# Optimization experiments

Measured on AMD Instinct MI355X. Metric: run time of the kernel, lower is better.

The kernel has to match this reference:

```python
import jax, jax.numpy as jnp
import numpy as np

B, T, D, HS = 4, 4096, 512, 64


def setup_inputs() -> dict:
    key = jax.random.key(0)
    kx, kd, kk, kq, kv = jax.random.split(key, 5)
    X = jax.random.normal(kx, (B, T, D), dtype=jnp.float32)
    dag = jax.random.randint(kd, (T, T), 0, 2, dtype=jnp.int32)
    scale = 1.0 / np.sqrt(D).astype(np.float32)
    Wk = jax.random.normal(kk, (D, HS), dtype=jnp.float32) * scale
    Wq = jax.random.normal(kq, (D, HS), dtype=jnp.float32) * scale
    Wv = jax.random.normal(kv, (D, HS), dtype=jnp.float32) * scale
    return {"X": X, "dag": dag, "Wk": Wk, "Wq": Wq, "Wv": Wv}


def reference(X, dag, Wk, Wq, Wv):
    # Projections (nn.Linear without bias): [B,T,HS]
    K = X @ Wk
    Q = X @ Wq
    V = X @ Wv
    hs = Q.shape[-1]
    # Dense scores [B,T,T]
    QK = jnp.einsum('bid,bjd->bij', Q, K) / np.float32(np.sqrt(hs))
    mask = (dag == 0)  # [T,T], True -> -inf
    # Rows fully masked would softmax to NaN in torch; the module zeroes them.
    row_dead = jnp.all(mask, axis=-1)  # [T]
    neg_inf = jnp.asarray(-jnp.inf, QK.dtype)
    scores = jnp.where(mask, neg_inf, QK)
    # Neutralize dead rows before softmax to avoid NaN, then zero them out
    scores = jnp.where(row_dead[:, None], jnp.zeros((), QK.dtype), scores)
    att = jax.nn.softmax(scores, axis=-1)
    att = jnp.where(row_dead[:, None], jnp.zeros((), att.dtype), att)
    # Transposed AV matmul: out[b,j,h] = sum_i att[b,i,j] * V[b,i,h]
    out = jnp.einsum('bij,bih->bjh', att, V)
    # Swish activation
    return out * jax.nn.sigmoid(out)
```

## Files before the change

kernel.cpp:

```cpp
#include <hip/hip_runtime.h>
#include <hip/hip_bf16.h>
#include <math.h>

#define BB 4
#define TT 4096
#define DD 512
#define HH 64
#define TW 128

typedef unsigned int u32;
typedef unsigned short u16;
typedef float f32x16 __attribute__((ext_vector_type(16)));
typedef __bf16 bf16x8 __attribute__((ext_vector_type(8)));

#define SC 0.18033688011112042f

static __device__ __forceinline__ u16 f2b(float f) {
    __hip_bfloat16 h = __float2bfloat16(f);
    return __builtin_bit_cast(u16, h);
}
static __device__ __forceinline__ float b2f(u16 x) {
    return __builtin_bit_cast(float, (u32)x << 16);
}
static __device__ __forceinline__ u32 pk2(float a, float b) {
    return (u32)f2b(a) | ((u32)f2b(b) << 16);
}
static __device__ __forceinline__ bf16x8 ldf(const u16* p) {
    uint4 u = *(const uint4*)p;
    return __builtin_bit_cast(bf16x8, u);
}
static __device__ __forceinline__ void swap32(u32& a, u32& b) {
    asm("v_permlane32_swap_b32 %0, %1" : "+v"(a), "+v"(b));
}


__global__ __launch_bounds__(256) void wtr_kernel(const float* __restrict__ Wq,
                                                  const float* __restrict__ Wk,
                                                  const float* __restrict__ Wv,
                                                  u16* __restrict__ Wt) {
    const int wb = blockIdx.x;
    const int m = wb >> 3, sub = wb & 7;
    const float* W = (m == 0) ? Wq : (m == 1) ? Wk : Wv;
    const int t = threadIdx.x;
    const int n = sub * 8 + (t >> 5);
    const int k0 = (t & 31) * 16;
    u16 buf[16];
#pragma unroll
    for (int k = 0; k < 16; ++k) buf[k] = f2b(W[(size_t)(k0 + k) * HH + n]);
    uint4* dst = (uint4*)(Wt + ((size_t)m * 64 + n) * DD + k0);
    dst[0] = *(uint4*)buf;
    dst[1] = *(uint4*)(buf + 8);
}

__global__ __launch_bounds__(384) void pp_kernel(const float* __restrict__ X,
                                                 const u16* __restrict__ Wt,
                                                 u16* __restrict__ QF,
                                                 u16* __restrict__ KF,
                                                 u16* __restrict__ VF,
                                                 const int* __restrict__ dag,
                                                 u32* __restrict__ bits2,
                                                 u32* __restrict__ bitsTT) {
    if (blockIdx.x >= 256) {
        const int w = threadIdx.x >> 6, lane = threadIdx.x & 63;
        const int unit = (blockIdx.x - 256) * 6 + w;
        if (unit >= 8192) return;
        const int i32r = unit >> 6;
        const int j64 = unit & 63;
        const int i0 = i32r * 32, j0 = j64 * 64;
        const int* p = dag + (size_t)i0 * TT + j0 + lane;
        u32* b2lo = bits2 + (size_t)(j64 * 2) * TT + i0;
        u32* b2hi = bits2 + (size_t)(j64 * 2 + 1) * TT + i0;
        int vals[32];
#pragma unroll
        for (int r = 0; r < 32; ++r) vals[r] = p[(size_t)r * TT];
        u32 colw = 0;
#pragma unroll
        for (int r = 0; r < 32; ++r) {
            unsigned long long m = __ballot(vals[r] != 0);
            colw |= (vals[r] != 0 ? 1u : 0u) << r;
            if (lane == 0) b2lo[r] = (u32)m;
            else if (lane == 32) b2hi[r] = (u32)(m >> 32);
        }
        bitsTT[(size_t)i32r * TT + j0 + lane] = colw;
        return;
    }
    const int w = threadIdx.x >> 6, lane = threadIdx.x & 63;
    const int m = w % 3, rg = w / 3;
    const int l31 = lane & 31, hf = lane >> 5;
    const int tile = blockIdx.x * 2 + rg;
    const int row0 = tile * 32;
    const float* xr = X + (size_t)(row0 + l31) * DD + hf * 8;
    const u16* wbase = Wt + (size_t)m * 64 * DD + hf * 8;

    f32x16 acc[2] = {};

    for (int kt = 0; kt < 32; ++kt) {
        float4 x0 = *(const float4*)(xr + kt * 16);
        float4 x1 = *(const float4*)(xr + kt * 16 + 4);
        uint4 aw;
        aw.x = pk2(x0.x, x0.y);
        aw.y = pk2(x0.z, x0.w);
        aw.z = pk2(x1.x, x1.y);
        aw.w = pk2(x1.z, x1.w);
        bf16x8 xa = __builtin_bit_cast(bf16x8, aw);
        const u16* wk = wbase + kt * 16;
#pragma unroll
        for (int nt = 0; nt < 2; ++nt) {
            bf16x8 wb = ldf(wk + (size_t)(nt * 32 + l31) * DD);
            acc[nt] = __builtin_amdgcn_mfma_f32_32x32x16_bf16(xa, wb, acc[nt], 0, 0, 0);
        }
    }
    const float sc = (m == 0) ? SC : 1.0f;
    if (m < 2) {
        u16* dst = (m == 0) ? QF : KF;
        const int kth = l31 >> 4, hfp = (l31 >> 3) & 1, e = l31 & 7;
#pragma unroll
        for (int nt = 0; nt < 2; ++nt)
#pragma unroll
            for (int r = 0; r < 16; ++r) {
                int rl = (r & 3) + 8 * (r >> 2) + 4 * hf;
                dst[(size_t)tile * 2048 + (nt * 2 + kth) * 512 + (rl + hfp * 32) * 8 + e]
                    = f2b(acc[nt][r] * sc);
            }
    } else {
#pragma unroll
        for (int nt = 0; nt < 2; ++nt)
#pragma unroll
            for (int r = 0; r < 16; ++r) {
                int rl = (r & 3) + 8 * (r >> 2) + 4 * hf;
                VF[(size_t)tile * 2048 + (nt * 2 + (rl >> 4)) * 512
                   + (l31 + ((rl >> 3) & 1) * 32) * 8 + (rl & 7)] = f2b(acc[nt][r]);
            }
    }
}

__global__ __launch_bounds__(512, 2) void stats_kernel(const u16* __restrict__ QF,
                                                       const u16* __restrict__ KF,
                                                       const u32* __restrict__ bits2,
                                                       const u16* __restrict__ VF,
                                                       u16* __restrict__ VF2) {
    __shared__ float Lsh[8][128];
    __shared__ float cSh[64];
    const int bid = blockIdx.x;
    const int b = (bid & 7) >> 1;
    const int u = (bid & 1) * 32 + (bid >> 3);
    const int itg0 = u * 2;
    const int i0 = itg0 * 32;
    const int w = threadIdx.x >> 6, lane = threadIdx.x & 63;
    const int l31 = lane & 31, hf = lane >> 5;

    bf16x8 qfA[4], qfB[4];
    const u16* qbase = QF + (size_t)(b * 128 + itg0) * 2048 + lane * 8;
#pragma unroll
    for (int kt = 0; kt < 4; ++kt) {
        qfA[kt] = ldf(qbase + kt * 512);
        qfB[kt] = ldf(qbase + 2048 + kt * 512);
    }

    const u16* kf0 = KF + (size_t)b * 128 * 2048 + lane * 8;

    float LpA = 0.f, LpB = 0.f;
    for (int t = 0; t < 16; ++t) {
        const int jt = w + t * 8;
        const u16* kb = kf0 + (size_t)jt * 2048;
        u32 mwA = bits2[(size_t)jt * TT + i0 + l31];
        u32 mwB = bits2[(size_t)jt * TT + i0 + 32 + l31];

        bf16x8 k0 = ldf(kb), k1 = ldf(kb + 512), k2 = ldf(kb + 1024), k3 = ldf(kb + 1536);
        __builtin_amdgcn_s_setprio(1);
        f32x16 sA = {}, sB = {};
        sA = __builtin_amdgcn_mfma_f32_32x32x16_bf16(k0, qfA[0], sA, 0, 0, 0);
        sB = __builtin_amdgcn_mfma_f32_32x32x16_bf16(k0, qfB[0], sB, 0, 0, 0);
        sA = __builtin_amdgcn_mfma_f32_32x32x16_bf16(k1, qfA[1], sA, 0, 0, 0);
        sB = __builtin_amdgcn_mfma_f32_32x32x16_bf16(k1, qfB[1], sB, 0, 0, 0);
        sA = __builtin_amdgcn_mfma_f32_32x32x16_bf16(k2, qfA[2], sA, 0, 0, 0);
        sB = __builtin_amdgcn_mfma_f32_32x32x16_bf16(k2, qfB[2], sB, 0, 0, 0);
        sA = __builtin_amdgcn_mfma_f32_32x32x16_bf16(k3, qfA[3], sA, 0, 0, 0);
        sB = __builtin_amdgcn_mfma_f32_32x32x16_bf16(k3, qfB[3], sB, 0, 0, 0);
        __builtin_amdgcn_s_setprio(0);
        u32 mrA = __builtin_amdgcn_alignbit(mwA, mwA, hf * 4);
        u32 mrB = __builtin_amdgcn_alignbit(mwB, mwB, hf * 4);
#pragma unroll
        for (int r = 0; r < 16; ++r) {
            const int pos = (r & 3) + 8 * (r >> 2);
            float eA = __builtin_amdgcn_exp2f(sA[r]);
            float eB = __builtin_amdgcn_exp2f(sB[r]);
            LpA += ((mrA >> pos) & 1) ? eA : 0.f;
            LpB += ((mrB >> pos) & 1) ? eB : 0.f;
        }
    }
    Lsh[w][lane] = LpA;
    Lsh[w][64 + lane] = LpB;
    __syncthreads();
    if (threadIdx.x < 64) {
        const int g = threadIdx.x >> 5, il = threadIdx.x & 31;
        float L = 0.f;
#pragma unroll
        for (int q = 0; q < 8; ++q) L += Lsh[q][g * 64 + il] + Lsh[q][g * 64 + il + 32];
        cSh[g * 32 + il] = (L > 0.f) ? 1.f / L : 0.f;
    }
    __syncthreads();
    {
        const int tl = threadIdx.x >> 8;
        const int rem = threadIdx.x & 255;
        const int q = rem >> 6, ln = rem & 63;
        const int ib = tl * 32 + (q & 1) * 16 + (ln >> 5) * 8;
        float4 c0 = *(const float4*)&cSh[ib];
        float4 c1 = *(const float4*)&cSh[ib + 4];
        const size_t off = (size_t)(b * 128 + itg0 + tl) * 2048 + q * 512 + ln * 8;
        uint4 v = *(const uint4*)(VF + off);
        u16* ve = (u16*)&v;
        ve[0] = f2b(b2f(ve[0]) * c0.x);
        ve[1] = f2b(b2f(ve[1]) * c0.y);
        ve[2] = f2b(b2f(ve[2]) * c0.z);
        ve[3] = f2b(b2f(ve[3]) * c0.w);
        ve[4] = f2b(b2f(ve[4]) * c1.x);
        ve[5] = f2b(b2f(ve[5]) * c1.y);
        ve[6] = f2b(b2f(ve[6]) * c1.z);
        ve[7] = f2b(b2f(ve[7]) * c1.w);
        *(uint4*)(VF2 + off) = v;
    }
}

__global__ __launch_bounds__(512, 2) void out_kernel(const u16* __restrict__ QF,
                                                     const u16* __restrict__ KF,
                                                     const u16* __restrict__ VF2,
                                                     const u32* __restrict__ bitsTT,
                                                     float* __restrict__ out) {
    __shared__ float red[2][4][2048];
    const int bid = blockIdx.x;
    const int b = (bid & 7) >> 1;
    const int u = (bid & 1) * 32 + (bid >> 3);
    const int jt0 = u * 2;
    const int j0 = jt0 * 32;
    const int w = threadIdx.x >> 6, lane = threadIdx.x & 63;
    const int l31 = lane & 31, hf = lane >> 5;

    bf16x8 kfA[4], kfB[4];
    const u16* kbase = KF + (size_t)(b * 128 + jt0) * 2048 + lane * 8;
#pragma unroll
    for (int kt = 0; kt < 4; ++kt) {
        kfA[kt] = ldf(kbase + kt * 512);
        kfB[kt] = ldf(kbase + 2048 + kt * 512);
    }

    const u16* qf0 = QF + (size_t)b * 128 * 2048 + lane * 8;
    const u16* vf0 = VF2 + (size_t)b * 128 * 2048 + lane * 8;

    f32x16 accA0 = {}, accA1 = {}, accB0 = {}, accB1 = {};

    for (int t = 0; t < 16; ++t) {
        const int it = w + t * 8;
        const u16* qb = qf0 + (size_t)it * 2048;
        const u16* vb = vf0 + (size_t)it * 2048;
        u32 mwA = bitsTT[(size_t)it * TT + j0 + l31];
        u32 mwB = bitsTT[(size_t)it * TT + j0 + 32 + l31];

        bf16x8 q0 = ldf(qb), q1 = ldf(qb + 512), q2 = ldf(qb + 1024), q3 = ldf(qb + 1536);
        __builtin_amdgcn_s_setprio(1);
        f32x16 sA = {}, sB = {};
        sA = __builtin_amdgcn_mfma_f32_32x32x16_bf16(q0, kfA[0], sA, 0, 0, 0);
        sB = __builtin_amdgcn_mfma_f32_32x32x16_bf16(q0, kfB[0], sB, 0, 0, 0);
        sA = __builtin_amdgcn_mfma_f32_32x32x16_bf16(q1, kfA[1], sA, 0, 0, 0);
        sB = __builtin_amdgcn_mfma_f32_32x32x16_bf16(q1, kfB[1], sB, 0, 0, 0);
        sA = __builtin_amdgcn_mfma_f32_32x32x16_bf16(q2, kfA[2], sA, 0, 0, 0);
        sB = __builtin_amdgcn_mfma_f32_32x32x16_bf16(q2, kfB[2], sB, 0, 0, 0);
        sA = __builtin_amdgcn_mfma_f32_32x32x16_bf16(q3, kfA[3], sA, 0, 0, 0);
        sB = __builtin_amdgcn_mfma_f32_32x32x16_bf16(q3, kfB[3], sB, 0, 0, 0);
        __builtin_amdgcn_s_setprio(0);

        u32 mrA = __builtin_amdgcn_alignbit(mwA, mwA, hf * 4);
        u32 mrB = __builtin_amdgcn_alignbit(mwB, mwB, hf * 4);

        float pA[16], pB[16];
#pragma unroll
        for (int r = 0; r < 16; ++r) {
            const int pos = (r & 3) + 8 * (r >> 2);
            float eA = __builtin_amdgcn_exp2f(sA[r]);
            float eB = __builtin_amdgcn_exp2f(sB[r]);
            pA[r] = ((mrA >> pos) & 1) ? eA : 0.f;
            pB[r] = ((mrB >> pos) & 1) ? eB : 0.f;
        }

        bf16x8 v00 = ldf(vb), v01 = ldf(vb + 512), v10 = ldf(vb + 1024), v11 = ldf(vb + 1536);

#pragma unroll
        for (int k2 = 0; k2 < 2; ++k2) {
            u32 aA  = pk2(pA[8 * k2 + 0], pA[8 * k2 + 1]);
            u32 bA  = pk2(pA[8 * k2 + 2], pA[8 * k2 + 3]);
            u32 cA  = pk2(pA[8 * k2 + 4], pA[8 * k2 + 5]);
            u32 dA  = pk2(pA[8 * k2 + 6], pA[8 * k2 + 7]);
            swap32(aA, cA);
            swap32(bA, dA);
            uint4 awA = {aA, bA, cA, dA};
            bf16x8 paA = __builtin_bit_cast(bf16x8, awA);
            u32 aB  = pk2(pB[8 * k2 + 0], pB[8 * k2 + 1]);
            u32 bB  = pk2(pB[8 * k2 + 2], pB[8 * k2 + 3]);
            u32 cB2 = pk2(pB[8 * k2 + 4], pB[8 * k2 + 5]);
            u32 dB  = pk2(pB[8 * k2 + 6], pB[8 * k2 + 7]);
            swap32(aB, cB2);
            swap32(bB, dB);
            uint4 awB = {aB, bB, cB2, dB};
            bf16x8 paB = __builtin_bit_cast(bf16x8, awB);
            bf16x8 v0 = (k2 == 0) ? v00 : v01;
            bf16x8 v1 = (k2 == 0) ? v10 : v11;
            __builtin_amdgcn_s_setprio(1);
            accA0 = __builtin_amdgcn_mfma_f32_32x32x16_bf16(paA, v0, accA0, 0, 0, 0);
            accB0 = __builtin_amdgcn_mfma_f32_32x32x16_bf16(paB, v0, accB0, 0, 0, 0);
            accA1 = __builtin_amdgcn_mfma_f32_32x32x16_bf16(paA, v1, accA1, 0, 0, 0);
            accB1 = __builtin_amdgcn_mfma_f32_32x32x16_bf16(paB, v1, accB1, 0, 0, 0);
            __builtin_amdgcn_s_setprio(0);
        }
    }

    if (w >= 4) {
#pragma unroll
        for (int r = 0; r < 16; ++r) {
            int jl = (r & 3) + 8 * (r >> 2) + 4 * hf;
            red[0][w - 4][jl * 64 + l31] = accA0[r];
            red[0][w - 4][jl * 64 + 32 + l31] = accA1[r];
            red[1][w - 4][jl * 64 + l31] = accB0[r];
            red[1][w - 4][jl * 64 + 32 + l31] = accB1[r];
        }
    }
    __syncthreads();
    if (w < 4) {
#pragma unroll
        for (int r = 0; r < 16; ++r) {
            int jl = (r & 3) + 8 * (r >> 2) + 4 * hf;
            red[0][w][jl * 64 + l31] += accA0[r];
            red[0][w][jl * 64 + 32 + l31] += accA1[r];
            red[1][w][jl * 64 + l31] += accB0[r];
            red[1][w][jl * 64 + 32 + l31] += accB1[r];
        }
    }
    __syncthreads();
    {
        const int idx = threadIdx.x * 8;
        const int g3 = idx >> 11, e = idx & 2047;
        float vv[8];
#pragma unroll
        for (int q = 0; q < 8; ++q) {
            int ee = e + q;
            float v = red[g3][0][ee] + red[g3][1][ee] + red[g3][2][ee] + red[g3][3][ee];
            vv[q] = v / (1.f + __expf(-v));
        }
        const int jl = e >> 6, hc = e & 63;
        float* dst = out + ((size_t)b * TT + (jt0 + g3) * 32 + jl) * HH + hc;
        *(float4*)dst = make_float4(vv[0], vv[1], vv[2], vv[3]);
        *(float4*)(dst + 4) = make_float4(vv[4], vv[5], vv[6], vv[7]);
    }
}

extern "C" void kernel_launch(void* const* d_in, const int* in_sizes, int n_in,
                              void* d_out, int out_size, void* d_ws, size_t ws_size,
                              hipStream_t stream) {
    const float* X  = (const float*)d_in[0];
    const int*  dag = (const int*)d_in[1];
    const float* Wk = (const float*)d_in[2];
    const float* Wq = (const float*)d_in[3];
    const float* Wv = (const float*)d_in[4];
    float* out = (float*)d_out;

    char* ws = (char*)d_ws;
    u16*   QF    = (u16*)ws;
    u16*   KF    = (u16*)(ws + (2u << 20));
    u16*   VF    = (u16*)(ws + (4u << 20));
    u16*   VF2   = (u16*)(ws + (6u << 20));
    u32*   bits2 = (u32*)(ws + (8u << 20));
    u32*   bitsTT= (u32*)(ws + (10u << 20));
    u16*   Wt    = (u16*)(ws + (12u << 20));

    wtr_kernel<<<24, 256, 0, stream>>>(Wq, Wk, Wv, Wt);
    pp_kernel<<<256 + 1366, 384, 0, stream>>>(X, Wt, QF, KF, VF, dag, bits2, bitsTT);
    stats_kernel<<<256, 512, 0, stream>>>(QF, KF, bits2, VF, VF2);
    out_kernel<<<256, 512, 0, stream>>>(QF, KF, VF2, bitsTT, out);
}
```

Measured before the change: 88.08 us.

## Pack dag bitmask with vectorized row reads and transpose in separate kernel

The dag-to-bitmask path in pp_kernel now reads each row with contiguous int4 loads, so each lane packs 32 consecutive columns into one word. This replaces the strided 32-row column reads and per-row ballots. The transposed mask bitsTT is no longer built there; a new trans_kernel builds it from bits2 using ballots. The goal is to cut uncoalesced global reads of the 64MB dag, at the cost of an extra kernel launch and a serial dependency before stats_kernel. The bits2 stores are now scattered 4-byte writes with stride TT.

```diff
diff --git a/kernel.cpp b/kernel.cpp
--- a/kernel.cpp
+++ b/kernel.cpp
@@ -58,30 +58,24 @@
                                                  u16* __restrict__ KF,
                                                  u16* __restrict__ VF,
                                                  const int* __restrict__ dag,
-                                                 u32* __restrict__ bits2,
-                                                 u32* __restrict__ bitsTT) {
+                                                 u32* __restrict__ bits2) {
     if (blockIdx.x >= 256) {
         const int w = threadIdx.x >> 6, lane = threadIdx.x & 63;
-        const int unit = (blockIdx.x - 256) * 6 + w;
-        if (unit >= 8192) return;
-        const int i32r = unit >> 6;
-        const int j64 = unit & 63;
-        const int i0 = i32r * 32, j0 = j64 * 64;
-        const int* p = dag + (size_t)i0 * TT + j0 + lane;
-        u32* b2lo = bits2 + (size_t)(j64 * 2) * TT + i0;
-        u32* b2hi = bits2 + (size_t)(j64 * 2 + 1) * TT + i0;
-        int vals[32];
-#pragma unroll
-        for (int r = 0; r < 32; ++r) vals[r] = p[(size_t)r * TT];
-        u32 colw = 0;
-#pragma unroll
-        for (int r = 0; r < 32; ++r) {
-            unsigned long long m = __ballot(vals[r] != 0);
-            colw |= (vals[r] != 0 ? 1u : 0u) << r;
-            if (lane == 0) b2lo[r] = (u32)m;
-            else if (lane == 32) b2hi[r] = (u32)(m >> 32);
-        }
-        bitsTT[(size_t)i32r * TT + j0 + lane] = colw;
+        const int row = (blockIdx.x - 256) * 3 + (w >> 1);
+        if (row >= TT) return;
+        const int h = w & 1;
+        const int c0 = h * 2048 + lane * 32;
+        const int* p = dag + (size_t)row * TT + c0;
+        u32 mk = 0;
+#pragma unroll
+        for (int q = 0; q < 8; ++q) {
+            int4 v = *(const int4*)(p + q * 4);
+            mk |= (v.x != 0 ? 1u : 0u) << (q * 4);
+            mk |= (v.y != 0 ? 1u : 0u) << (q * 4 + 1);
+            mk |= (v.z != 0 ? 1u : 0u) << (q * 4 + 2);
+            mk |= (v.w != 0 ? 1u : 0u) << (q * 4 + 3);
+        }
+        bits2[(size_t)(h * 64 + lane) * TT + row] = mk;
         return;
     }
     const int w = threadIdx.x >> 6, lane = threadIdx.x & 63;
@@ -132,6 +126,24 @@
                    + (l31 + ((rl >> 3) & 1) * 32) * 8 + (rl & 7)] = f2b(acc[nt][r]);
             }
     }
+}
+
+__global__ __launch_bounds__(256) void trans_kernel(const u32* __restrict__ bits2,
+                                                    u32* __restrict__ bitsTT) {
+    const int w = threadIdx.x >> 6, lane = threadIdx.x & 63;
+    const int l31 = lane & 31, grp = lane >> 5;
+    const int g = blockIdx.x * 8 + w * 2 + grp;
+    const int it = g >> 7, jt = g & 127;
+    u32 S = bits2[(size_t)jt * TT + it * 32 + l31];
+    u32 sel = 0;
+    const bool low = (lane < 32);
+#pragma unroll
+    for (int jb = 0; jb < 32; ++jb) {
+        unsigned long long m = __ballot((S >> jb) & 1);
+        u32 pick = low ? (u32)m : (u32)(m >> 32);
+        sel = (l31 == jb) ? pick : sel;
+    }
+    bitsTT[(size_t)it * TT + jt * 32 + l31] = sel;
 }
 
 __global__ __launch_bounds__(512, 2) void stats_kernel(const u16* __restrict__ QF,
@@ -372,7 +384,8 @@
     u16*   Wt    = (u16*)(ws + (12u << 20));
 
     wtr_kernel<<<24, 256, 0, stream>>>(Wq, Wk, Wv, Wt);
-    pp_kernel<<<256 + 1366, 384, 0, stream>>>(X, Wt, QF, KF, VF, dag, bits2, bitsTT);
+    pp_kernel<<<256 + 1366, 384, 0, stream>>>(X, Wt, QF, KF, VF, dag, bits2);
+    trans_kernel<<<2048, 256, 0, stream>>>(bits2, bitsTT);
     stats_kernel<<<256, 512, 0, stream>>>(QF, KF, bits2, VF, VF2);
     out_kernel<<<256, 512, 0, stream>>>(QF, KF, VF2, bitsTT, out);
 }
```

Measured after the change: 98.48 us. 11.8% more time.
